# Kernel tuning notes

Measured on AMD Instinct MI355X. Metric: run time of the kernel, lower is better.

## Reference

```python
import jax, jax.numpy as jnp
import numpy as np
from jax import lax

RATIO = 0.25
RADIUS = 0.2
K = 64  # max_num_neighbors


def _fps(xyz, S):
    """Farthest point sampling, start at index 0 (pytorch3d default). xyz: [B,N,3] -> [B,S] int32."""
    B, N, _ = xyz.shape
    init_idx = jnp.zeros((B,), jnp.int32)
    init_mind = jnp.full((B, N), 1e10, dtype=xyz.dtype)

    def body(carry, _):
        min_d, last_idx = carry
        last = jnp.take_along_axis(xyz, last_idx[:, None, None], axis=1)  # [B,1,3]
        d = jnp.sum((xyz - last) ** 2, axis=-1)  # [B,N]
        min_d = jnp.minimum(min_d, d)
        nxt = jnp.argmax(min_d, axis=-1).astype(jnp.int32)
        return (min_d, nxt), nxt

    (_, _), rest = lax.scan(body, (init_mind, init_idx), None, length=S - 1)  # rest: [S-1,B]
    return jnp.concatenate([init_idx[None, :], rest], axis=0).T  # [B,S]


def _ball_query(new_xyz, xyz, radius, k):
    """First-k neighbors of each query within radius, -1 padded (pytorch3d semantics).
    new_xyz: [B,S,3], xyz: [B,N,3] -> idx [B,S,k] int32."""
    N = xyz.shape[1]
    d2 = jnp.sum((new_xyz[:, :, None, :] - xyz[:, None, :, :]) ** 2, axis=-1)  # [B,S,N]
    within = d2 < radius * radius
    keys = jnp.where(within, jnp.arange(N, dtype=jnp.int32), jnp.int32(N))  # [B,S,N]
    neg_top, _ = lax.top_k(-keys, k)  # smallest k keys (first-in-order neighbors)
    sel = -neg_top  # ascending original indices, N = padding
    return jnp.where(sel < N, sel, jnp.int32(-1))


def _gather(points, idx):
    """points [B,N,C], idx [B,S,Kn] -> [B,S,Kn,C]."""
    B, S, Kn = idx.shape
    C = points.shape[-1]
    flat = jnp.take_along_axis(points, idx.reshape(B, S * Kn, 1), axis=1)
    return flat.reshape(B, S, Kn, C)


def setup_inputs() -> dict:
    key = jax.random.key(0)
    ks = jax.random.split(key, 8)
    B, N, D = 8, 4096, 64
    c_in, h, c_out = 3 + D, 64, 128
    x = jax.random.normal(ks[0], (B, N, D), dtype=jnp.float32)
    pos = jax.random.uniform(ks[1], (B, N, 3), dtype=jnp.float32)
    W1 = jax.random.normal(ks[2], (c_in, h), dtype=jnp.float32) / np.sqrt(c_in)
    b1 = jnp.zeros((h,), jnp.float32)
    W2 = jax.random.normal(ks[3], (h, h), dtype=jnp.float32) / np.sqrt(h)
    b2 = jnp.zeros((h,), jnp.float32)
    W3 = jax.random.normal(ks[4], (h, c_out), dtype=jnp.float32) / np.sqrt(h)
    b3 = jnp.zeros((c_out,), jnp.float32)
    return {"x": x, "pos": pos, "W1": W1, "b1": b1, "W2": W2, "b2": b2, "W3": W3, "b3": b3}


def reference(x, pos, W1, b1, W2, b2, W3, b3):
    B, N, C = pos.shape
    S = int(RATIO * N)
    # sample_and_group
    fps_idx = _fps(pos, S)  # [B,S]
    new_xyz = jnp.take_along_axis(pos, fps_idx[:, :, None], axis=1)  # [B,S,3]
    idx = _ball_query(new_xyz, pos, RADIUS, K)  # [B,S,K]
    mask = idx != -1
    idx_safe = jnp.where(idx < 0, N - 1, idx)  # torch points[-1] == last point
    grouped_xyz = _gather(pos, idx_safe)  # [B,S,K,3]
    grouped_xyz_norm = grouped_xyz - new_xyz[:, :, None, :]
    grouped_pts = _gather(x, idx_safe)  # [B,S,K,D]
    new_points = jnp.concatenate([grouped_xyz_norm, grouped_pts], axis=-1)  # [B,S,K,3+D]
    # shared pointwise MLP (self.conv)
    hdn = jax.nn.relu(new_points @ W1 + b1)
    hdn = jax.nn.relu(hdn @ W2 + b2)
    hdn = hdn @ W3 + b3  # [B,S,K,128]
    # masked max-pool over neighbors
    hdn = hdn * mask[..., None].astype(hdn.dtype)
    out = jnp.max(hdn, axis=2)  # [B,S,128]
    return out, new_xyz
```

## Files before the change

### kernel.cpp

```cpp
#include <hip/hip_runtime.h>
#include <stdint.h>

#define NB 8
#define NP 4096
#define NS 1024
#define NK 64
#define ND 64
#define NH 64
#define NCO 128

#define FPS_T 512
#define PPT (NP / FPS_T)

#define K1P 104
#define K2P 72

#define WS_WIDX 0
#define WS_WT   32768

typedef _Float16 half8v __attribute__((ext_vector_type(8)));
typedef _Float16 half4v __attribute__((ext_vector_type(4)));
typedef _Float16 half2v __attribute__((ext_vector_type(2)));
typedef float    floatx4 __attribute__((ext_vector_type(4)));

template <int CTRL>
__device__ __forceinline__ float dpp_mov_f32(float x) {
    return __int_as_float(__builtin_amdgcn_update_dpp(
        0, __float_as_int(x), CTRL, 0xf, 0xf, true));
}

__global__ __launch_bounds__(64) void wt_kernel(const float* __restrict__ W1,
                                                const float* __restrict__ W2,
                                                const float* __restrict__ W3,
                                                _Float16* __restrict__ wt)
{
    const int j = blockIdx.x;
    const int t = threadIdx.x;
    if (j < 64) {
        for (int k = t; k < K1P; k += 64) {
            float v = 0.f;
            if (k < 64)       v = W1[(3 + k) * 64 + j];
            else if (k < 67)  v = W1[(k - 64) * 64 + j];
            wt[j * K1P + k] = (_Float16)v;
        }
    } else if (j < 128) {
        const int r = j - 64;
        for (int k = t; k < K2P; k += 64) {
            float v = (k < 64) ? W2[k * 64 + r] : 0.f;
            wt[6656 + r * K2P + k] = (_Float16)v;
        }
    } else {
        const int r = j - 128;
        for (int k = t; k < K2P; k += 64) {
            float v = (k < 64) ? W3[k * 128 + r] : 0.f;
            wt[11264 + r * K2P + k] = (_Float16)v;
        }
    }
}

__global__ __launch_bounds__(512, 2) void fused_kernel(
        const float* __restrict__ x, const float* __restrict__ pos,
        const float* __restrict__ b1v, const float* __restrict__ b2v,
        const float* __restrict__ b3v,
        const _Float16* __restrict__ wt,
        float* __restrict__ new_xyz, float* __restrict__ out, int* widx)
{
    __shared__ alignas(16) char smem[65664];
    const int tid  = threadIdx.x;
    const int lane = tid & 63;
    const int wv   = tid >> 6;

    if (blockIdx.x < NB) {
#pragma clang fp contract(off)
        const int b = blockIdx.x;
        float4* sp = (float4*)smem;
        unsigned long long* kbuf = (unsigned long long*)(smem + 65536);

        const float* p = pos + (size_t)b * NP * 3;
        for (int i = tid; i < NP; i += FPS_T) {
            sp[i] = make_float4(p[i * 3 + 0], p[i * 3 + 1], p[i * 3 + 2], 0.0f);
        }
        __syncthreads();

        float px[PPT], py[PPT], pz[PPT], md[PPT];
#pragma unroll
        for (int j = 0; j < PPT; ++j) {
            float4 v = sp[tid * PPT + j];
            px[j] = v.x; py[j] = v.y; pz[j] = v.z;
            md[j] = 1e10f;
        }

        int last = 0;
        if (tid == 0) {
            __hip_atomic_store(widx + b * NS, 0, __ATOMIC_RELAXED,
                               __HIP_MEMORY_SCOPE_AGENT);
        }
        int tok = 0;

        int par = 0;
        for (int s = 1; s < NS; ++s) {
            const float4 lp = sp[last];
            const float lx = lp.x, ly = lp.y, lz = lp.z;

            float bv = 0.0f;
            int   bi = tid * PPT;
#pragma unroll
            for (int j = 0; j < PPT; ++j) {
                float dx = px[j] - lx;
                float dy = py[j] - ly;
                float dz = pz[j] - lz;
                float d2 = dx * dx + dy * dy + dz * dz;
                float m  = (md[j] < d2) ? md[j] : d2;
                md[j] = m;
                if (m > bv) { bv = m; bi = tid * PPT + j; }
            }

            float r = bv;
            r = fmaxf(r, dpp_mov_f32<0x111>(r));
            r = fmaxf(r, dpp_mov_f32<0x112>(r));
            r = fmaxf(r, dpp_mov_f32<0x114>(r));
            r = fmaxf(r, dpp_mov_f32<0x118>(r));
            r = fmaxf(r, dpp_mov_f32<0x142>(r));
            r = fmaxf(r, dpp_mov_f32<0x143>(r));
            const float gmax = __int_as_float(
                __builtin_amdgcn_readlane(__float_as_int(r), 63));

            unsigned long long mk = __ballot(bv == gmax);
            int wl = (int)__builtin_ctzll(mk);
            int bw = __builtin_amdgcn_readlane(bi, wl);

            if (lane == 0) {
                kbuf[par * 8 + wv] =
                    ((unsigned long long)__float_as_uint(gmax) << 32) |
                    (unsigned long long)(~(unsigned)bw);
            }
            __syncthreads();

            const ulonglong2* wb = (const ulonglong2*)(kbuf + par * 8);
            ulonglong2 q0 = wb[0], q1 = wb[1], q2 = wb[2], q3 = wb[3];
            unsigned long long a0 = (q0.y > q0.x) ? q0.y : q0.x;
            unsigned long long a1 = (q1.y > q1.x) ? q1.y : q1.x;
            unsigned long long a2 = (q2.y > q2.x) ? q2.y : q2.x;
            unsigned long long a3 = (q3.y > q3.x) ? q3.y : q3.x;
            unsigned long long b0 = (a1 > a0) ? a1 : a0;
            unsigned long long b1 = (a3 > a2) ? a3 : a2;
            unsigned long long g  = (b1 > b0) ? b1 : b0;

            last = (int)(~(unsigned)g);

            if ((s & 15) == lane) tok = last;
            if ((s & 15) == 15 && wv == 0 && lane < 16) {
                __hip_atomic_store(widx + b * NS + (s - 15) + lane, tok,
                                   __ATOMIC_RELAXED, __HIP_MEMORY_SCOPE_AGENT);
            }
            par ^= 1;
        }
        return;
    }

    const int ci = blockIdx.x - NB;
    const int b  = ci & 7;
    const int r0 = ci >> 3;

    _Float16* G   = (_Float16*)smem;
    _Float16* H1  = (_Float16*)(smem + 13312);
    _Float16* H2  = (_Float16*)(smem + 22528);
    float*    CW  = (float*)(smem + 31744);
    float*    Lb  = (float*)(smem + 33792);
    short*  nbr_s = (short*)(smem + 34304);
    float*    qv  = (float*)(smem + 34432);

    const int qd = lane >> 4;
    const int c  = lane & 15;
    const int myrow = wv * 16 + c;

    half8v a1[3][4], a2[2][4], a3[2][8];
    float b3r = 0.f;
    if (tid < 256) {
#pragma unroll
        for (int ks = 0; ks < 3; ++ks)
#pragma unroll
            for (int mt = 0; mt < 4; ++mt)
                a1[ks][mt] = *(const half8v*)&wt[(mt * 16 + c) * K1P + ks * 32 + qd * 8];
#pragma unroll
        for (int ks = 0; ks < 2; ++ks)
#pragma unroll
            for (int mt = 0; mt < 4; ++mt)
                a2[ks][mt] = *(const half8v*)&wt[6656 + (mt * 16 + c) * K2P + ks * 32 + qd * 8];
#pragma unroll
        for (int ks = 0; ks < 2; ++ks)
#pragma unroll
            for (int mt = 0; mt < 8; ++mt)
                a3[ks][mt] = *(const half8v*)&wt[11264 + (mt * 16 + c) * K2P + ks * 32 + qd * 8];
        if (tid < 64) { Lb[tid] = b1v[tid]; Lb[64 + tid] = b2v[tid]; }
        if (tid < NCO) b3r = b3v[tid];
        half8v z = {};
        for (int i = tid; i < (64 * K1P) / 8; i += 256) ((half8v*)G)[i] = z;
    }

    for (int s = r0; s < NS; s += 31) {
        const int bs = b * NS + s;

        int idx = -1, guard = 0;
        for (;;) {
            idx = __hip_atomic_load(widx + bs, __ATOMIC_RELAXED,
                                    __HIP_MEMORY_SCOPE_AGENT);
            if (idx >= 0) break;
            __builtin_amdgcn_s_sleep(8);
            if (++guard > (1 << 26)) break;
        }
        const int qidx = (idx >= 0 && idx < NP) ? idx : 0;

        if (wv == 0) {
#pragma clang fp contract(off)
            const float* p = pos + (size_t)b * NP * 3;
            const float qx = p[qidx * 3 + 0];
            const float qy = p[qidx * 3 + 1];
            const float qz = p[qidx * 3 + 2];
            if (lane == 0) {
                qv[0] = qx; qv[1] = qy; qv[2] = qz;
                float* o = new_xyz + (size_t)bs * 3;
                o[0] = qx; o[1] = qy; o[2] = qz;
            }
            int cnt = 0;
            for (int n0 = 0; n0 < NP; n0 += 64) {
                const int n = n0 + lane;
                float dx = qx - p[n * 3 + 0];
                float dy = qy - p[n * 3 + 1];
                float dz = qz - p[n * 3 + 2];
                float d2 = dx * dx + dy * dy + dz * dz;
                bool within = d2 < 0.04f;
                unsigned long long m = __ballot(within);
                if (within) {
                    int slot = cnt + __popcll(m & ((1ull << lane) - 1ull));
                    if (slot < NK) nbr_s[slot] = (short)n;
                }
                cnt += (int)__popcll(m);
                if (cnt >= NK) break;
            }
            if (cnt < NK) {
                if (lane < NK - cnt) nbr_s[cnt + lane] = (short)-1;
            }
        }
        __syncthreads();

        if (tid < 256) {
            const int ni = tid >> 2;
            const int p4 = tid & 3;
            const int n  = (int)nbr_s[ni];
            const int nn = (n < 0) ? (NP - 1) : n;
            const float* xr = x + ((size_t)b * NP + nn) * ND + p4 * 16;
#pragma unroll
            for (int i = 0; i < 4; ++i) {
                float4 v = *(const float4*)(xr + 4 * i);
                half4v h;
                h[0] = (_Float16)v.x; h[1] = (_Float16)v.y;
                h[2] = (_Float16)v.z; h[3] = (_Float16)v.w;
                *(half4v*)&G[ni * K1P + p4 * 16 + 4 * i] = h;
            }
            if (p4 == 0) {
                const float* pr = pos + (size_t)(b * NP + nn) * 3;
                float gx = pr[0] - qv[0];
                float gy = pr[1] - qv[1];
                float gz = pr[2] - qv[2];
                half2v h2; h2[0] = (_Float16)gx; h2[1] = (_Float16)gy;
                *(half2v*)&G[ni * K1P + 64] = h2;
                G[ni * K1P + 66] = (_Float16)gz;
            }
        }
        __syncthreads();

        if (tid < 256) {
            {
                floatx4 acc[4] = {};
#pragma unroll
                for (int ks = 0; ks < 3; ++ks) {
                    half8v bf = *(const half8v*)&G[myrow * K1P + ks * 32 + qd * 8];
#pragma unroll
                    for (int mt = 0; mt < 4; ++mt)
                        acc[mt] = __builtin_amdgcn_mfma_f32_16x16x32_f16(a1[ks][mt], bf, acc[mt], 0, 0, 0);
                }
#pragma unroll
                for (int mt = 0; mt < 4; ++mt) {
                    float4 bb = *(const float4*)&Lb[mt * 16 + qd * 4];
                    half4v h;
                    h[0] = (_Float16)fmaxf(acc[mt][0] + bb.x, 0.f);
                    h[1] = (_Float16)fmaxf(acc[mt][1] + bb.y, 0.f);
                    h[2] = (_Float16)fmaxf(acc[mt][2] + bb.z, 0.f);
                    h[3] = (_Float16)fmaxf(acc[mt][3] + bb.w, 0.f);
                    *(half4v*)&H1[myrow * K2P + mt * 16 + qd * 4] = h;
                }
            }
            {
                floatx4 acc[4] = {};
#pragma unroll
                for (int ks = 0; ks < 2; ++ks) {
                    half8v bf = *(const half8v*)&H1[myrow * K2P + ks * 32 + qd * 8];
#pragma unroll
                    for (int mt = 0; mt < 4; ++mt)
                        acc[mt] = __builtin_amdgcn_mfma_f32_16x16x32_f16(a2[ks][mt], bf, acc[mt], 0, 0, 0);
                }
#pragma unroll
                for (int mt = 0; mt < 4; ++mt) {
                    float4 bb = *(const float4*)&Lb[64 + mt * 16 + qd * 4];
                    half4v h;
                    h[0] = (_Float16)fmaxf(acc[mt][0] + bb.x, 0.f);
                    h[1] = (_Float16)fmaxf(acc[mt][1] + bb.y, 0.f);
                    h[2] = (_Float16)fmaxf(acc[mt][2] + bb.z, 0.f);
                    h[3] = (_Float16)fmaxf(acc[mt][3] + bb.w, 0.f);
                    *(half4v*)&H2[myrow * K2P + mt * 16 + qd * 4] = h;
                }
            }
            {
                floatx4 acc3[8] = {};
#pragma unroll
                for (int ks = 0; ks < 2; ++ks) {
                    half8v av = *(const half8v*)&H2[myrow * K2P + ks * 32 + qd * 8];
#pragma unroll
                    for (int mt = 0; mt < 8; ++mt)
                        acc3[mt] = __builtin_amdgcn_mfma_f32_16x16x32_f16(av, a3[ks][mt], acc3[mt], 0, 0, 0);
                }
                const short* np4 = &nbr_s[wv * 16 + qd * 4];
                const bool v0 = np4[0] >= 0, v1 = np4[1] >= 0;
                const bool v2 = np4[2] >= 0, v3 = np4[3] >= 0;
#pragma unroll
                for (int mt = 0; mt < 8; ++mt) {
                    float m = v0 ? acc3[mt][0] : -INFINITY;
                    m = fmaxf(m, v1 ? acc3[mt][1] : -INFINITY);
                    m = fmaxf(m, v2 ? acc3[mt][2] : -INFINITY);
                    m = fmaxf(m, v3 ? acc3[mt][3] : -INFINITY);
                    m = fmaxf(m, __shfl_xor(m, 16));
                    m = fmaxf(m, __shfl_xor(m, 32));
                    if (qd == 0) CW[wv * NCO + mt * 16 + c] = m;
                }
            }
        }
        __syncthreads();

        if (tid < NCO) {
            float m = fmaxf(fmaxf(CW[tid], CW[NCO + tid]),
                            fmaxf(CW[2 * NCO + tid], CW[3 * NCO + tid]));
            m += b3r;
            if (nbr_s[NK - 1] < 0) m = fmaxf(m, 0.f);
            out[(size_t)bs * NCO + tid] = m;
        }
        __syncthreads();
    }
}

extern "C" void kernel_launch(void* const* d_in, const int* in_sizes, int n_in,
                              void* d_out, int out_size, void* d_ws, size_t ws_size,
                              hipStream_t stream) {
    const float* x   = (const float*)d_in[0];
    const float* pos = (const float*)d_in[1];
    const float* W1  = (const float*)d_in[2];
    const float* b1  = (const float*)d_in[3];
    const float* W2  = (const float*)d_in[4];
    const float* b2  = (const float*)d_in[5];
    const float* W3  = (const float*)d_in[6];
    const float* b3  = (const float*)d_in[7];

    float* out0 = (float*)d_out;
    float* nxyz = out0 + (size_t)NB * NS * NCO;
    int*      widxp = (int*)((char*)d_ws + WS_WIDX);
    _Float16* wtp   = (_Float16*)((char*)d_ws + WS_WT);

    wt_kernel<<<256, 64, 0, stream>>>(W1, W2, W3, wtp);
    fused_kernel<<<256, 512, 0, stream>>>(x, pos, b1, b2, b3, wtp,
                                          nxyz, out0, widxp);
}
```

Before: 754.9 us.

## Fold weight transpose into fused kernel and pack FPS distance math into float2

Removes the separate weight-transposition kernel launch. Each consumer block now converts W1/W2/W3 to fp16 in shared memory itself, then loads its MFMA operand registers from there. The FPS inner loop now computes distances on float2 pairs, which can map to packed FP32 instructions. It also replaces the running argmax with a max tree followed by a first-index select. This trades one launch and a global round trip for redundant per-block weight conversion work.

```diff
diff --git a/kernel.cpp b/kernel.cpp
--- a/kernel.cpp
+++ b/kernel.cpp
@@ -16,12 +16,12 @@
 #define K2P 72
 
 #define WS_WIDX 0
-#define WS_WT   32768
-
-typedef _Float16 half8v __attribute__((ext_vector_type(8)));
-typedef _Float16 half4v __attribute__((ext_vector_type(4)));
-typedef _Float16 half2v __attribute__((ext_vector_type(2)));
+
+typedef _Float16 half8v  __attribute__((ext_vector_type(8)));
+typedef _Float16 half4v  __attribute__((ext_vector_type(4)));
+typedef _Float16 half2v  __attribute__((ext_vector_type(2)));
 typedef float    floatx4 __attribute__((ext_vector_type(4)));
+typedef float    floatx2 __attribute__((ext_vector_type(2)));
 
 template <int CTRL>
 __device__ __forceinline__ float dpp_mov_f32(float x) {
@@ -29,40 +29,11 @@
         0, __float_as_int(x), CTRL, 0xf, 0xf, true));
 }
 
-__global__ __launch_bounds__(64) void wt_kernel(const float* __restrict__ W1,
-                                                const float* __restrict__ W2,
-                                                const float* __restrict__ W3,
-                                                _Float16* __restrict__ wt)
-{
-    const int j = blockIdx.x;
-    const int t = threadIdx.x;
-    if (j < 64) {
-        for (int k = t; k < K1P; k += 64) {
-            float v = 0.f;
-            if (k < 64)       v = W1[(3 + k) * 64 + j];
-            else if (k < 67)  v = W1[(k - 64) * 64 + j];
-            wt[j * K1P + k] = (_Float16)v;
-        }
-    } else if (j < 128) {
-        const int r = j - 64;
-        for (int k = t; k < K2P; k += 64) {
-            float v = (k < 64) ? W2[k * 64 + r] : 0.f;
-            wt[6656 + r * K2P + k] = (_Float16)v;
-        }
-    } else {
-        const int r = j - 128;
-        for (int k = t; k < K2P; k += 64) {
-            float v = (k < 64) ? W3[k * 128 + r] : 0.f;
-            wt[11264 + r * K2P + k] = (_Float16)v;
-        }
-    }
-}
-
 __global__ __launch_bounds__(512, 2) void fused_kernel(
         const float* __restrict__ x, const float* __restrict__ pos,
-        const float* __restrict__ b1v, const float* __restrict__ b2v,
-        const float* __restrict__ b3v,
-        const _Float16* __restrict__ wt,
+        const float* __restrict__ W1, const float* __restrict__ b1v,
+        const float* __restrict__ W2, const float* __restrict__ b2v,
+        const float* __restrict__ W3, const float* __restrict__ b3v,
         float* __restrict__ new_xyz, float* __restrict__ out, int* widx)
 {
     __shared__ alignas(16) char smem[65664];
@@ -82,12 +53,15 @@
         }
         __syncthreads();
 
-        float px[PPT], py[PPT], pz[PPT], md[PPT];
-#pragma unroll
-        for (int j = 0; j < PPT; ++j) {
-            float4 v = sp[tid * PPT + j];
-            px[j] = v.x; py[j] = v.y; pz[j] = v.z;
-            md[j] = 1e10f;
+        floatx2 px2[4], py2[4], pz2[4], md2[4];
+#pragma unroll
+        for (int pr = 0; pr < 4; ++pr) {
+            float4 v0 = sp[tid * PPT + 2 * pr];
+            float4 v1 = sp[tid * PPT + 2 * pr + 1];
+            px2[pr][0] = v0.x; px2[pr][1] = v1.x;
+            py2[pr][0] = v0.y; py2[pr][1] = v1.y;
+            pz2[pr][0] = v0.z; pz2[pr][1] = v1.z;
+            md2[pr][0] = 1e10f; md2[pr][1] = 1e10f;
         }
 
         int last = 0;
@@ -100,20 +74,29 @@
         int par = 0;
         for (int s = 1; s < NS; ++s) {
             const float4 lp = sp[last];
-            const float lx = lp.x, ly = lp.y, lz = lp.z;
-
-            float bv = 0.0f;
-            int   bi = tid * PPT;
-#pragma unroll
-            for (int j = 0; j < PPT; ++j) {
-                float dx = px[j] - lx;
-                float dy = py[j] - ly;
-                float dz = pz[j] - lz;
-                float d2 = dx * dx + dy * dy + dz * dz;
-                float m  = (md[j] < d2) ? md[j] : d2;
-                md[j] = m;
-                if (m > bv) { bv = m; bi = tid * PPT + j; }
-            }
+            const floatx2 lxv = {lp.x, lp.x};
+            const floatx2 lyv = {lp.y, lp.y};
+            const floatx2 lzv = {lp.z, lp.z};
+
+            float m[8];
+#pragma unroll
+            for (int pr = 0; pr < 4; ++pr) {
+                floatx2 dx = px2[pr] - lxv;
+                floatx2 dy = py2[pr] - lyv;
+                floatx2 dz = pz2[pr] - lzv;
+                floatx2 d2 = dx * dx + dy * dy + dz * dz;
+                float m0 = (md2[pr][0] < d2[0]) ? md2[pr][0] : d2[0];
+                float m1 = (md2[pr][1] < d2[1]) ? md2[pr][1] : d2[1];
+                md2[pr][0] = m0; md2[pr][1] = m1;
+                m[2 * pr] = m0; m[2 * pr + 1] = m1;
+            }
+            float bv = fmaxf(fmaxf(fmaxf(m[0], m[1]), fmaxf(m[2], m[3])),
+                             fmaxf(fmaxf(m[4], m[5]), fmaxf(m[6], m[7])));
+            int jsel = 0;
+#pragma unroll
+            for (int j = 7; j >= 0; --j)
+                jsel = (m[j] == bv) ? j : jsel;
+            int bi = tid * PPT + jsel;
 
             float r = bv;
             r = fmaxf(r, dpp_mov_f32<0x111>(r));
@@ -162,6 +145,52 @@
     const int b  = ci & 7;
     const int r0 = ci >> 3;
 
+    _Float16* sWt = (_Float16*)smem;
+
+    {
+        const int j = tid & 63;
+        for (int k = tid >> 6; k < K1P; k += 8) {
+            float v = 0.f;
+            if (k < 64)      v = W1[(3 + k) * 64 + j];
+            else if (k < 67) v = W1[(k - 64) * 64 + j];
+            sWt[j * K1P + k] = (_Float16)v;
+        }
+        for (int k = tid >> 6; k < K2P; k += 8) {
+            float v = (k < 64) ? W2[k * 64 + j] : 0.f;
+            sWt[6656 + j * K2P + k] = (_Float16)v;
+        }
+        const int r = tid & 127;
+        for (int k = tid >> 7; k < K2P; k += 4) {
+            float v = (k < 64) ? W3[k * 128 + r] : 0.f;
+            sWt[11264 + r * K2P + k] = (_Float16)v;
+        }
+    }
+    __syncthreads();
+
+    const int qd = lane >> 4;
+    const int c  = lane & 15;
+    const int myrow = wv * 16 + c;
+
+    half8v a1[3][4], a2[2][4], a3[2][8];
+    if (tid < 256) {
+#pragma unroll
+        for (int ks = 0; ks < 3; ++ks)
+#pragma unroll
+            for (int mt = 0; mt < 4; ++mt)
+                a1[ks][mt] = *(const half8v*)&sWt[(mt * 16 + c) * K1P + ks * 32 + qd * 8];
+#pragma unroll
+        for (int ks = 0; ks < 2; ++ks)
+#pragma unroll
+            for (int mt = 0; mt < 4; ++mt)
+                a2[ks][mt] = *(const half8v*)&sWt[6656 + (mt * 16 + c) * K2P + ks * 32 + qd * 8];
+#pragma unroll
+        for (int ks = 0; ks < 2; ++ks)
+#pragma unroll
+            for (int mt = 0; mt < 8; ++mt)
+                a3[ks][mt] = *(const half8v*)&sWt[11264 + (mt * 16 + c) * K2P + ks * 32 + qd * 8];
+    }
+    __syncthreads();
+
     _Float16* G   = (_Float16*)smem;
     _Float16* H1  = (_Float16*)(smem + 13312);
     _Float16* H2  = (_Float16*)(smem + 22528);
@@ -170,28 +199,8 @@
     short*  nbr_s = (short*)(smem + 34304);
     float*    qv  = (float*)(smem + 34432);
 
-    const int qd = lane >> 4;
-    const int c  = lane & 15;
-    const int myrow = wv * 16 + c;
-
-    half8v a1[3][4], a2[2][4], a3[2][8];
     float b3r = 0.f;
     if (tid < 256) {
-#pragma unroll
-        for (int ks = 0; ks < 3; ++ks)
-#pragma unroll
-            for (int mt = 0; mt < 4; ++mt)
-                a1[ks][mt] = *(const half8v*)&wt[(mt * 16 + c) * K1P + ks * 32 + qd * 8];
-#pragma unroll
-        for (int ks = 0; ks < 2; ++ks)
-#pragma unroll
-            for (int mt = 0; mt < 4; ++mt)
-                a2[ks][mt] = *(const half8v*)&wt[6656 + (mt * 16 + c) * K2P + ks * 32 + qd * 8];
-#pragma unroll
-        for (int ks = 0; ks < 2; ++ks)
-#pragma unroll
-            for (int mt = 0; mt < 8; ++mt)
-                a3[ks][mt] = *(const half8v*)&wt[11264 + (mt * 16 + c) * K2P + ks * 32 + qd * 8];
         if (tid < 64) { Lb[tid] = b1v[tid]; Lb[64 + tid] = b2v[tid]; }
         if (tid < NCO) b3r = b3v[tid];
         half8v z = {};
@@ -362,10 +371,8 @@
 
     float* out0 = (float*)d_out;
     float* nxyz = out0 + (size_t)NB * NS * NCO;
-    int*      widxp = (int*)((char*)d_ws + WS_WIDX);
-    _Float16* wtp   = (_Float16*)((char*)d_ws + WS_WT);
-
-    wt_kernel<<<256, 64, 0, stream>>>(W1, W2, W3, wtp);
-    fused_kernel<<<256, 512, 0, stream>>>(x, pos, b1, b2, b3, wtp,
+    int*   widxp = (int*)((char*)d_ws + WS_WIDX);
+
+    fused_kernel<<<256, 512, 0, stream>>>(x, pos, W1, b1, W2, b2, W3, b3,
                                           nxyz, out0, widxp);
 }
```

New measurement: 768.5 us. About the same (+1.8%).
